# Optimization experiments

Hardware: AMD Instinct MI355X
Metric: run time of the kernel (lower is better)

Reference implementation:

```python
import jax, jax.numpy as jnp
import numpy as np
import math

LOG2 = math.log(2)
M, D, E, H = 65536, 768, 20, 64
PAIR = 3 * D + 2 * E  # mem, mention, hadamard + distance/counter feature embs


def get_bucket(count):
    """Identity buckets for count<=4, log2 buckets above, clamped to [0, 9]."""
    c = count.astype(jnp.int32)
    logspace = jnp.floor(jnp.log(jnp.maximum(c, 1).astype(jnp.float32)) / LOG2).astype(jnp.int32) + 3
    idx = jnp.where(c <= 4, c, logspace)
    return jnp.clip(idx, 0, 9)


def setup_inputs() -> dict:
    key = jax.random.key(0)
    ks = jax.random.split(key, 8)
    ment_emb = jax.random.normal(ks[0], (D,), jnp.float32)
    mem_vectors = jax.random.normal(ks[1], (M, D), jnp.float32)
    ent_counter = jax.random.randint(ks[2], (M,), 0, 50).astype(jnp.int32)
    last_mention_start = jax.random.randint(ks[3], (M,), 0, 50000).astype(jnp.int32)
    dist_table = jax.random.normal(ks[4], (10, E), jnp.float32)
    counter_table = jax.random.normal(ks[5], (10, E), jnp.float32)
    W1 = jax.random.normal(ks[6], (PAIR, H), jnp.float32) / np.sqrt(PAIR)
    b1 = jnp.zeros((H,), jnp.float32)
    W2 = jax.random.normal(ks[7], (H, 1), jnp.float32) / np.sqrt(H)
    b2 = jnp.zeros((1,), jnp.float32)
    return dict(ment_emb=ment_emb, mem_vectors=mem_vectors, dist_table=dist_table,
                counter_table=counter_table, W1=W1, b1=b1, W2=W2, b2=b2,
                ent_counter=ent_counter, last_mention_start=last_mention_start,
                ment_start=50000)


def reference(ment_emb, mem_vectors, dist_table, counter_table, W1, b1, W2, b2,
              ent_counter, last_mention_start, ment_start):
    # Feature embeddings: bucketized distance + bucketized entity counter lookups
    dist = ment_start - last_mention_start                      # [M]
    dist_embs = dist_table[get_bucket(dist)]                    # [M, E]
    cnt_embs = counter_table[get_bucket(ent_counter)]           # [M, E]
    feature_embs = jnp.concatenate([dist_embs, cnt_embs], axis=-1)  # [M, 2E]

    # Pair vector: [mem, mention (repeated), mem*mention, features]
    rep = jnp.broadcast_to(ment_emb, mem_vectors.shape)         # [M, D]
    pair = jnp.concatenate([mem_vectors, rep, mem_vectors * rep, feature_embs], axis=-1)  # [M, PAIR]

    # Small scoring MLP (1 hidden layer, ReLU); dropout is identity at eval
    h = jax.nn.relu(pair @ W1 + b1)                             # [M, H]
    score = (h @ W2 + b2)[:, 0]                                 # [M]

    # Append dummy new-cluster score 0, mask empty cluster slots with -10000
    mask = jnp.concatenate([(ent_counter > 0).astype(jnp.float32), jnp.ones((1,), jnp.float32)])
    score = jnp.concatenate([score, jnp.zeros((1,), jnp.float32)])
    coref_new_score = score * mask + (1.0 - mask) * (-10000.0)  # [M+1]
    return coref_new_score
```

## Files before the change

### kernel.cpp

```cpp
#include <hip/hip_runtime.h>
#include <hip/hip_bf16.h>

#define MROWS 65536
#define DD 768
#define HH 64

typedef __attribute__((ext_vector_type(8))) short short8;
typedef __attribute__((ext_vector_type(4))) float f32x4;

__device__ inline unsigned short f2bf(float x) {
    union { float f; unsigned u; } v; v.f = x;
    unsigned r = v.u + 0x7fffu + ((v.u >> 16) & 1u);
    return (unsigned short)(r >> 16);
}

__device__ inline int bucket(int c) {
    int idx = (c <= 4) ? c : (34 - __clz(c));
    idx = idx < 0 ? 0 : idx;
    return idx > 9 ? 9 : idx;
}

__global__ __launch_bounds__(1024) void precompute_kernel(
                                  const float* __restrict__ ment,
                                  const float* __restrict__ dist_t,
                                  const float* __restrict__ cnt_t,
                                  const float* __restrict__ W1,
                                  const float* __restrict__ b1,
                                  unsigned short* __restrict__ Wf,
                                  float* __restrict__ constv,
                                  float* __restrict__ dlut,
                                  float* __restrict__ clut) {
    __shared__ float red[1024];
    int b = blockIdx.x;
    if (b < 24) {
        int s = b;
        for (int e = threadIdx.x; e < 2048; e += blockDim.x) {
            int t    = e >> 9;
            int lane = (e >> 3) & 63;
            int j    = e & 7;
            int d = s * 32 + ((j >> 2) << 4) + (((lane >> 4) & 3) << 2) + (j & 3);
            int h = t * 16 + (lane & 15);
            float v = W1[d * HH + h] + ment[d] * W1[(1536 + d) * HH + h];
            Wf[(size_t)((s * 4 + t) * 64 + lane) * 8 + j] = f2bf(v);
        }
    } else if (b == 24) {
        int h = threadIdx.x & 63;
        int chunk = threadIdx.x >> 6;
        float acc = 0.f;
        #pragma unroll 8
        for (int d = chunk * 48; d < chunk * 48 + 48; ++d)
            acc += ment[d] * W1[(768 + d) * HH + h];
        red[threadIdx.x] = acc;
        __syncthreads();
        if (chunk == 0) {
            float s0 = b1[h];
            #pragma unroll
            for (int k = 0; k < 16; ++k) s0 += red[k * 64 + h];
            constv[h] = s0;
        }
    } else if (b == 25) {
        for (int e = threadIdx.x; e < 640; e += blockDim.x) {
            int tt = e >> 6, h = e & 63;
            float a = 0.f;
            #pragma unroll
            for (int k = 0; k < 20; ++k)
                a += dist_t[tt * 20 + k] * W1[(2304 + k) * HH + h];
            dlut[e] = a;
        }
    } else if (b == 26) {
        for (int e = threadIdx.x; e < 640; e += blockDim.x) {
            int tt = e >> 6, h = e & 63;
            float a = 0.f;
            #pragma unroll
            for (int k = 0; k < 20; ++k)
                a += cnt_t[tt * 20 + k] * W1[(2324 + k) * HH + h];
            clut[e] = a;
        }
    }
}

__global__ __launch_bounds__(256) void score_kernel(
    const float* __restrict__ mem,
    const unsigned short* __restrict__ Wf,
    const float* __restrict__ constv,
    const float* __restrict__ dlut,
    const float* __restrict__ clut,
    const float* __restrict__ W2,
    const float* __restrict__ b2p,
    const int* __restrict__ entc,
    const int* __restrict__ lms,
    const int* __restrict__ msp,
    float* __restrict__ out) {

    int wave = threadIdx.x >> 6;
    int lane = threadIdx.x & 63;
    int g  = lane >> 4;
    int c0 = lane & 15;
    int row0 = blockIdx.x * 64 + wave * 16;

    if (blockIdx.x == 0 && threadIdx.x == 0) out[MROWS] = 0.0f;

    const float* arow = mem + (size_t)(row0 + c0) * DD + g * 4;

    f32x4 acc0 = {0.f,0.f,0.f,0.f}, acc1 = {0.f,0.f,0.f,0.f};
    f32x4 acc2 = {0.f,0.f,0.f,0.f}, acc3 = {0.f,0.f,0.f,0.f};

    #pragma unroll 4
    for (int s = 0; s < 24; ++s) {
        f32x4 a0 = *(const f32x4*)(arow + s * 32);
        f32x4 a1 = *(const f32x4*)(arow + s * 32 + 16);
        short8 af;
        af[0] = (short)f2bf(a0[0]); af[1] = (short)f2bf(a0[1]);
        af[2] = (short)f2bf(a0[2]); af[3] = (short)f2bf(a0[3]);
        af[4] = (short)f2bf(a1[0]); af[5] = (short)f2bf(a1[1]);
        af[6] = (short)f2bf(a1[2]); af[7] = (short)f2bf(a1[3]);

        const unsigned short* bp = Wf + (size_t)s * 2048 + lane * 8;
        short8 bf0 = *(const short8*)(bp);
        short8 bf1 = *(const short8*)(bp + 512);
        short8 bf2 = *(const short8*)(bp + 1024);
        short8 bf3 = *(const short8*)(bp + 1536);

        acc0 = __builtin_amdgcn_mfma_f32_16x16x32_bf16(af, bf0, acc0, 0, 0, 0);
        acc1 = __builtin_amdgcn_mfma_f32_16x16x32_bf16(af, bf1, acc1, 0, 0, 0);
        acc2 = __builtin_amdgcn_mfma_f32_16x16x32_bf16(af, bf2, acc2, 0, 0, 0);
        acc3 = __builtin_amdgcn_mfma_f32_16x16x32_bf16(af, bf3, acc3, 0, 0, 0);
    }

    int ms  = msp[0];
    float b2v = b2p[0];
    float cv[4], w2[4];
    #pragma unroll
    for (int t = 0; t < 4; ++t) {
        cv[t] = constv[t * 16 + c0];
        w2[t] = W2[t * 16 + c0];
    }

    #pragma unroll
    for (int i = 0; i < 4; ++i) {
        int row = row0 + g * 4 + i;
        int c    = entc[row];
        int dist = ms - lms[row];
        int db = bucket(dist);
        int cb = bucket(c);
        float part = 0.f;
        #pragma unroll
        for (int t = 0; t < 4; ++t) {
            float a = (t == 0) ? acc0[i] : (t == 1) ? acc1[i] : (t == 2) ? acc2[i] : acc3[i];
            int hc = t * 16 + c0;
            float h = a + cv[t] + dlut[db * 64 + hc] + clut[cb * 64 + hc];
            h = fmaxf(h, 0.f);
            part += h * w2[t];
        }
        part += __shfl_xor(part, 8, 64);
        part += __shfl_xor(part, 4, 64);
        part += __shfl_xor(part, 2, 64);
        part += __shfl_xor(part, 1, 64);
        if (c0 == 0)
            out[row] = (c > 0) ? (part + b2v) : -10000.0f;
    }
}

extern "C" void kernel_launch(void* const* d_in, const int* in_sizes, int n_in,
                              void* d_out, int out_size, void* d_ws, size_t ws_size,
                              hipStream_t stream) {
    const float* ment   = (const float*)d_in[0];
    const float* mem    = (const float*)d_in[1];
    const float* dist_t = (const float*)d_in[2];
    const float* cnt_t  = (const float*)d_in[3];
    const float* W1     = (const float*)d_in[4];
    const float* b1     = (const float*)d_in[5];
    const float* W2     = (const float*)d_in[6];
    const float* b2     = (const float*)d_in[7];
    const int*   entc   = (const int*)d_in[8];
    const int*   lmsp   = (const int*)d_in[9];
    const int*   msp    = (const int*)d_in[10];

    unsigned short* Wf = (unsigned short*)d_ws;
    float* constv = (float*)((char*)d_ws + 98304);
    float* dlut   = constv + 64;
    float* clut   = dlut + 640;

    precompute_kernel<<<27, 1024, 0, stream>>>(ment, dist_t, cnt_t, W1, b1, Wf, constv, dlut, clut);
    score_kernel<<<1024, 256, 0, stream>>>(mem, Wf, constv, dlut, clut, W2, b2,
                                           entc, lmsp, msp, (float*)d_out);
}
```

Before: 48.38 us.

## Stage A tiles through swizzled LDS with software-pipelined global loads

The score kernel now has each wave load its 16x128-float slice of mem_vectors with fully coalesced 16-byte row-contiguous loads into registers. It writes these into a double-buffered, XOR-swizzled LDS region per wave, then reads the MFMA A-fragments back from LDS. Loads for the next chunk of A and B are issued ahead of the MFMAs on the current chunk in a hand-unrolled pipeline. This targets the strided, poorly coalesced direct global reads of the old layout and the load-latency stalls. The cost is 64KB of LDS per block, heavy register use for the staging buffers, and a launch bound of 2 blocks that limits occupancy.

```diff
diff --git a/kernel.cpp b/kernel.cpp
--- a/kernel.cpp
+++ b/kernel.cpp
@@ -79,7 +79,50 @@
     }
 }
 
-__global__ __launch_bounds__(256) void score_kernel(
+
+#define GLOADA(RBUF, S) do {                                            \
+    _Pragma("unroll")                                                   \
+    for (int t = 0; t < 8; ++t)                                         \
+        RBUF[t] = *(const f32x4*)(gA + (size_t)t * 6144 + (size_t)(S) * 512); \
+} while (0)
+
+#define GLOADB(BBUF, H) do {                                            \
+    _Pragma("unroll")                                                   \
+    for (int n = 0; n < 4; ++n) {                                       \
+        BBUF[n]     = *(const short8*)(bpl + (size_t)(2 * (H)) * 2048 + n * 512);     \
+        BBUF[4 + n] = *(const short8*)(bpl + (size_t)(2 * (H) + 1) * 2048 + n * 512); \
+    }                                                                   \
+} while (0)
+
+#define DSWRITE(RBUF, S) do {                                           \
+    char* wb_ = ldsb + (((S) & 1) << 13);                               \
+    _Pragma("unroll")                                                   \
+    for (int t = 0; t < 8; ++t) {                                       \
+        int row_ = 2 * t + subrow2;                                     \
+        *(f32x4*)(wb_ + row_ * 512 + ((piece16) ^ ((row_ & 7) << 4))) = RBUF[t]; \
+    }                                                                   \
+} while (0)
+
+#define COMP2(S, P, BBUF) do {                                          \
+    const char* rb_ = ldsb + (((S) & 1) << 13);                         \
+    _Pragma("unroll")                                                   \
+    for (int s2 = 0; s2 < 2; ++s2) {                                    \
+        int sp_ = 2 * (P) + s2;                                         \
+        f32x4 a0 = *(const f32x4*)(rb_ + rowb + ((sp_ * 128 + g16) ^ key));      \
+        f32x4 a1 = *(const f32x4*)(rb_ + rowb + ((sp_ * 128 + 64 + g16) ^ key)); \
+        short8 af;                                                      \
+        af[0] = (short)f2bf(a0[0]); af[1] = (short)f2bf(a0[1]);         \
+        af[2] = (short)f2bf(a0[2]); af[3] = (short)f2bf(a0[3]);         \
+        af[4] = (short)f2bf(a1[0]); af[5] = (short)f2bf(a1[1]);         \
+        af[6] = (short)f2bf(a1[2]); af[7] = (short)f2bf(a1[3]);         \
+        acc[0] = __builtin_amdgcn_mfma_f32_16x16x32_bf16(af, BBUF[s2 * 4 + 0], acc[0], 0, 0, 0); \
+        acc[1] = __builtin_amdgcn_mfma_f32_16x16x32_bf16(af, BBUF[s2 * 4 + 1], acc[1], 0, 0, 0); \
+        acc[2] = __builtin_amdgcn_mfma_f32_16x16x32_bf16(af, BBUF[s2 * 4 + 2], acc[2], 0, 0, 0); \
+        acc[3] = __builtin_amdgcn_mfma_f32_16x16x32_bf16(af, BBUF[s2 * 4 + 3], acc[3], 0, 0, 0); \
+    }                                                                   \
+} while (0)
+
+__global__ __launch_bounds__(256, 2) void score_kernel(
     const float* __restrict__ mem,
     const unsigned short* __restrict__ Wf,
     const float* __restrict__ constv,
@@ -92,6 +135,8 @@
     const int* __restrict__ msp,
     float* __restrict__ out) {
 
+    __shared__ __align__(16) char lds_raw[4][16384];
+
     int wave = threadIdx.x >> 6;
     int lane = threadIdx.x & 63;
     int g  = lane >> 4;
@@ -100,32 +145,40 @@
 
     if (blockIdx.x == 0 && threadIdx.x == 0) out[MROWS] = 0.0f;
 
-    const float* arow = mem + (size_t)(row0 + c0) * DD + g * 4;
-
-    f32x4 acc0 = {0.f,0.f,0.f,0.f}, acc1 = {0.f,0.f,0.f,0.f};
-    f32x4 acc2 = {0.f,0.f,0.f,0.f}, acc3 = {0.f,0.f,0.f,0.f};
-
-    #pragma unroll 4
-    for (int s = 0; s < 24; ++s) {
-        f32x4 a0 = *(const f32x4*)(arow + s * 32);
-        f32x4 a1 = *(const f32x4*)(arow + s * 32 + 16);
-        short8 af;
-        af[0] = (short)f2bf(a0[0]); af[1] = (short)f2bf(a0[1]);
-        af[2] = (short)f2bf(a0[2]); af[3] = (short)f2bf(a0[3]);
-        af[4] = (short)f2bf(a1[0]); af[5] = (short)f2bf(a1[1]);
-        af[6] = (short)f2bf(a1[2]); af[7] = (short)f2bf(a1[3]);
-
-        const unsigned short* bp = Wf + (size_t)s * 2048 + lane * 8;
-        short8 bf0 = *(const short8*)(bp);
-        short8 bf1 = *(const short8*)(bp + 512);
-        short8 bf2 = *(const short8*)(bp + 1024);
-        short8 bf3 = *(const short8*)(bp + 1536);
-
-        acc0 = __builtin_amdgcn_mfma_f32_16x16x32_bf16(af, bf0, acc0, 0, 0, 0);
-        acc1 = __builtin_amdgcn_mfma_f32_16x16x32_bf16(af, bf1, acc1, 0, 0, 0);
-        acc2 = __builtin_amdgcn_mfma_f32_16x16x32_bf16(af, bf2, acc2, 0, 0, 0);
-        acc3 = __builtin_amdgcn_mfma_f32_16x16x32_bf16(af, bf3, acc3, 0, 0, 0);
-    }
+    char* ldsb = &lds_raw[wave][0];
+
+    int subrow2 = lane >> 5;
+    int piece16 = (lane & 31) * 16;
+    const char* gA = (const char*)mem + (size_t)(row0 + subrow2) * 3072 + (lane & 31) * 16;
+
+    unsigned key  = (unsigned)((c0 & 7) << 4);
+    unsigned rowb = (unsigned)(c0 * 512);
+    unsigned g16  = (unsigned)(g * 16);
+
+    const unsigned short* bpl = Wf + lane * 8;
+
+    f32x4 acc[4];
+    #pragma unroll
+    for (int t = 0; t < 4; ++t) acc[t] = (f32x4){0.f, 0.f, 0.f, 0.f};
+
+    f32x4 rA[8], rB[8];
+    short8 bA[8], bB[8];
+
+    GLOADA(rA, 0); GLOADB(bA, 0);
+    DSWRITE(rA, 0);
+    GLOADA(rB, 1); GLOADB(bB, 1);
+
+    COMP2(0, 0, bA); GLOADB(bA, 2);  COMP2(0, 1, bB); DSWRITE(rB, 1);
+    GLOADA(rA, 2);   GLOADB(bB, 3);
+    COMP2(1, 0, bA); GLOADB(bA, 4);  COMP2(1, 1, bB); DSWRITE(rA, 2);
+    GLOADA(rB, 3);   GLOADB(bB, 5);
+    COMP2(2, 0, bA); GLOADB(bA, 6);  COMP2(2, 1, bB); DSWRITE(rB, 3);
+    GLOADA(rA, 4);   GLOADB(bB, 7);
+    COMP2(3, 0, bA); GLOADB(bA, 8);  COMP2(3, 1, bB); DSWRITE(rA, 4);
+    GLOADA(rB, 5);   GLOADB(bB, 9);
+    COMP2(4, 0, bA); GLOADB(bA, 10); COMP2(4, 1, bB); DSWRITE(rB, 5);
+    GLOADB(bB, 11);
+    COMP2(5, 0, bA);                 COMP2(5, 1, bB);
 
     int ms  = msp[0];
     float b2v = b2p[0];
@@ -146,7 +199,7 @@
         float part = 0.f;
         #pragma unroll
         for (int t = 0; t < 4; ++t) {
-            float a = (t == 0) ? acc0[i] : (t == 1) ? acc1[i] : (t == 2) ? acc2[i] : acc3[i];
+            float a = acc[t][i];
             int hc = t * 16 + c0;
             float h = a + cv[t] + dlut[db * 64 + hc] + clut[cb * 64 + hc];
             h = fmaxf(h, 0.f);
```

Result: faster. 45.29 us (-6.4%).
